# Performance work log

Measured on AMD Instinct MI355X. Metric: run time of the kernel, lower is better.

The kernel has to match this reference:

```python
import jax, jax.numpy as jnp
import numpy as np

N, E, L = 2048, 16384, 8
IN_DIM, HID, PE, EDGE_DIM, OUT_DIM, HEADS, MASK_DIM = 9, 256, 20, 2, 6, 8, 6
ENC = HID - PE
HD = HID // HEADS

def _bn(x, g, b):
    # BatchNorm1d in training-mode math (batch statistics, biased var), dropout disabled
    mu = x.mean(0)
    var = ((x - mu) ** 2).mean(0)
    return (x - mu) * jax.lax.rsqrt(var + 1e-5) * g + b

def _leaky(x):
    return jnp.where(x > 0, x, 0.01 * x)

def setup_inputs():
    key = jax.random.key(0)
    ks = iter(jax.random.split(key, 64))
    def p(*shape):
        return jax.random.normal(next(ks), shape, jnp.float32) * 0.05
    return dict(
        x=jax.random.normal(next(ks), (N, IN_DIM), jnp.float32),
        pe=jax.random.normal(next(ks), (N, PE), jnp.float32),
        edge_attr=jax.random.normal(next(ks), (E, EDGE_DIM), jnp.float32),
        mask_value=jax.random.normal(next(ks), (MASK_DIM,), jnp.float32),
        enc_w=p(IN_DIM, ENC), enc_b=p(ENC),
        in_g=jnp.ones((ENC,)), in_b=jnp.zeros((ENC,)),
        pe_g=jnp.ones((PE,)), pe_b=jnp.zeros((PE,)),
        gine_ew=p(L, EDGE_DIM, HID), gine_eb=p(L, HID),
        gine_mw=p(L, HID, HID), gine_mb=p(L, HID),
        attn_inw=p(L, HID, 3 * HID), attn_inb=p(L, 3 * HID),
        attn_outw=p(L, HID, HID), attn_outb=p(L, HID),
        mlp1w=p(L, HID, 2 * HID), mlp1b=p(L, 2 * HID),
        mlp2w=p(L, 2 * HID, HID), mlp2b=p(L, HID),
        n1g=jnp.ones((L, HID)), n1b=jnp.zeros((L, HID)),
        n2g=jnp.ones((L, HID)), n2b=jnp.zeros((L, HID)),
        n3g=jnp.ones((L, HID)), n3b=jnp.zeros((L, HID)),
        obn_g=jnp.ones((L, HID)), obn_b=jnp.zeros((L, HID)),
        pd_g=jnp.ones((HID,)), pd_b=jnp.zeros((HID,)),
        dec1w=p(HID, HID), dec1b=p(HID),
        dec2w=p(HID, OUT_DIM), dec2b=p(OUT_DIM),
        edge_index=jax.random.randint(next(ks), (2, E), 0, N, jnp.int32),
        mask=jax.random.randint(next(ks), (N, MASK_DIM), 0, 2, jnp.int32).astype(bool),
    )

def reference(x, pe, edge_attr, mask_value, enc_w, enc_b, in_g, in_b, pe_g, pe_b,
              gine_ew, gine_eb, gine_mw, gine_mb, attn_inw, attn_inb, attn_outw, attn_outb,
              mlp1w, mlp1b, mlp2w, mlp2b, n1g, n1b, n2g, n2b, n3g, n3b, obn_g, obn_b,
              pd_g, pd_b, dec1w, dec1b, dec2w, dec2b, edge_index, mask):
    src, dst = edge_index[0], edge_index[1]
    # masked-feature replacement on x[:, 3:3+mask_dim]
    blk = jnp.where(mask, mask_value[None, :], x[:, 3:3 + MASK_DIM])
    x = x.at[:, 3:3 + MASK_DIM].set(blk)
    h = _bn(_leaky(x @ enc_w + enc_b), in_g, in_b)
    h = jnp.concatenate([h, _bn(pe, pe_g, pe_b)], axis=1)  # [N, HID]
    for l in range(L):
        xin = h
        # GINEConv (eps=0): nn((1+eps)*x_i + sum_j relu(x_j + lin(e_ji)))
        eemb = edge_attr @ gine_ew[l] + gine_eb[l]            # [E, HID]
        msg = jax.nn.relu(xin[src] + eemb)                    # gather + fuse
        agg = jax.ops.segment_sum(msg, dst, num_segments=N)   # scatter-add
        hl = _leaky((xin + agg) @ gine_mw[l] + gine_mb[l])
        hl = _bn(hl + xin, n1g[l], n1b[l])                    # local branch + residual + norm1
        # global multi-head self-attention (single graph -> dense batch, no padding)
        qkv = xin @ attn_inw[l] + attn_inb[l]
        q, k, v = [t.reshape(N, HEADS, HD) for t in jnp.split(qkv, 3, axis=1)]
        a = jax.nn.softmax(jnp.einsum('nhd,mhd->hnm', q, k) / np.float32(np.sqrt(HD)), axis=-1)
        o = jnp.einsum('hnm,mhd->nhd', a, v).reshape(N, HID)
        ha = _bn(o @ attn_outw[l] + attn_outb[l] + xin, n2g[l], n2b[l])  # attn branch + residual + norm2
        out = hl + ha
        out = out + (jax.nn.relu(out @ mlp1w[l] + mlp1b[l]) @ mlp2w[l] + mlp2b[l])  # GPS FFN
        out = _bn(out, n3g[l], n3b[l])
        h = _bn(out, obn_g[l], obn_b[l])                      # outer per-layer BatchNorm
    h = _bn(h, pd_g, pd_b)
    return _leaky(h @ dec1w + dec1b) @ dec2w + dec2b
```

## Files before the change

### kernel.cpp

```cpp
#include <hip/hip_runtime.h>
#include <hip/hip_bf16.h>

typedef __hip_bfloat16 bf16;
typedef __attribute__((ext_vector_type(8))) short v8s;
typedef __attribute__((ext_vector_type(4))) float v4f;

#define NN 2048
#define EE 16384
#define LLAYERS 8
#define HIDD 256
#define ENCD 236
#define PED 20
#define BN_EPS 1e-5f
#define ATT_SCALE_L2E (0.17677669529663687f * 1.4426950408889634f)
#define KSPLIT 4

__device__ __forceinline__ float b2f(bf16 v){ return __bfloat162float(v); }
__device__ __forceinline__ float bs2f(unsigned short u){ return __uint_as_float(((unsigned)u) << 16); }
__device__ __forceinline__ unsigned short f2bs(float f){
  bf16 h = __float2bfloat16(f);
  union { bf16 b; unsigned short u; } cv; cv.b = h; return cv.u;
}
__device__ __forceinline__ float ld1f(const void* p, size_t i, int f){
  return f ? b2f(((const bf16*)p)[i]) : ((const float*)p)[i];
}

__global__ void k_detect2(const unsigned int* __restrict__ xw,
                          const unsigned char* __restrict__ mk, int* __restrict__ flags){
  __shared__ int sh[256];
  int t = threadIdx.x;
  if (blockIdx.x == 0){
    int cnt = 0;
    for (int i = t; i < 8192; i += 256){
      unsigned b = (xw[i] >> 8) & 0xffu;
      unsigned v = b & 0x7fu;
      if (v == 0u || (v >= 0x30u && v <= 0x43u)) cnt++;
    }
    sh[t] = cnt; __syncthreads();
    for (int s = 128; s; s >>= 1){ if (t < s) sh[t] += sh[t+s]; __syncthreads(); }
    if (t == 0) flags[0] = (sh[0] > 6000) ? 1 : 0;
  } else {
    int acc = 0;
    for (int i = t; i < NN*6; i += 256){
      unsigned b = mk[i]; int m = i & 3;
      if ((m == 1 && b == 0x3Fu) || (m == 0 && b == 0x80u)) acc |= 4;
      if (b == 0x3Fu || b == 0x80u) acc |= 2;
      if (m != 0 && b != 0u) acc |= 1;
    }
    sh[t] = acc; __syncthreads();
    for (int s = 128; s; s >>= 1){ if (t < s) sh[t] |= sh[t+s]; __syncthreads(); }
    if (t == 0){
      int a = sh[0];
      flags[1] = (a & 4) ? 2 : (a & 2) ? 3 : (a & 1) ? 1 : 0;
    }
  }
}

__global__ void k_tw(const void* __restrict__ src, unsigned short* __restrict__ dst,
                     int K, int N, const int* __restrict__ dflag){
  __shared__ float tile[32][33];
  int n0 = blockIdx.x*32, k0 = blockIdx.y*32, b = blockIdx.z;
  int t = threadIdx.x, x = t & 31, y = t >> 5;
  int f = dflag[0];
  size_t so = (size_t)b*K*N, dofs = (size_t)b*N*K;
  #pragma unroll
  for (int i = 0; i < 4; i++){
    int k = k0 + y + 8*i;
    tile[y+8*i][x] = ld1f(src, so + (size_t)k*N + n0 + x, f);
  }
  __syncthreads();
  #pragma unroll
  for (int i = 0; i < 4; i++){
    int n = n0 + y + 8*i;
    dst[dofs + (size_t)n*K + k0 + x] = f2bs(tile[x][y+8*i]);
  }
}
__global__ void k_tw3(const void* __restrict__ sA, const void* __restrict__ sB,
                      const void* __restrict__ sC, unsigned short* __restrict__ dst,
                      const int* __restrict__ dflag){
  __shared__ float tile[32][33];
  int z = blockIdx.z;
  const void* src = (z < 8) ? sA : (z < 16) ? sB : sC;
  int b = (z < 8) ? z : (z < 16) ? z - 8 : 0;
  int n0 = blockIdx.x*32, k0 = blockIdx.y*32;
  int t = threadIdx.x, x = t & 31, y = t >> 5;
  int f = dflag[0];
  size_t so = (size_t)b*65536, dofs = (size_t)z*65536;
  #pragma unroll
  for (int i = 0; i < 4; i++){
    int k = k0 + y + 8*i;
    tile[y+8*i][x] = ld1f(src, so + (size_t)k*256 + n0 + x, f);
  }
  __syncthreads();
  #pragma unroll
  for (int i = 0; i < 4; i++){
    int n = n0 + y + 8*i;
    dst[dofs + (size_t)n*256 + k0 + x] = f2bs(tile[x][y+8*i]);
  }
}

__global__ void k_csr_count(const int* __restrict__ ei, int* __restrict__ counts){
  int e = blockIdx.x*256 + threadIdx.x;
  if (e < EE) atomicAdd(&counts[ei[EE + e]], 1);
}
__global__ void k_csr_scan(const int* __restrict__ counts, int* __restrict__ rowstart,
                           int* __restrict__ cursor){
  __shared__ int ts[256];
  int t = threadIdx.x, base = t*8;
  int loc[8]; int s = 0;
  #pragma unroll
  for (int i = 0; i < 8; i++){ loc[i] = s; s += counts[base + i]; }
  ts[t] = s; __syncthreads();
  for (int off = 1; off < 256; off <<= 1){
    int v = (t >= off) ? ts[t - off] : 0;
    __syncthreads();
    ts[t] += v;
    __syncthreads();
  }
  int excl = ts[t] - s;
  #pragma unroll
  for (int i = 0; i < 8; i++){
    int v = excl + loc[i];
    rowstart[base + i] = v; cursor[base + i] = v;
  }
  if (t == 255) rowstart[2048] = ts[255];
}
__global__ void k_csr_fill(const int* __restrict__ ei, const void* __restrict__ ea,
                           const int* __restrict__ dflag, int* __restrict__ cursor,
                           int* __restrict__ csr_src, float2* __restrict__ csr_a){
  int e = blockIdx.x*256 + threadIdx.x;
  if (e >= EE) return;
  int s = ei[e], d = ei[EE + e];
  int pos = atomicAdd(&cursor[d], 1);
  int f = dflag[0];
  csr_src[pos] = s;
  csr_a[pos] = make_float2(ld1f(ea, (size_t)e*2, f), ld1f(ea, (size_t)e*2 + 1, f));
}

__global__ void k_encode(const void* __restrict__ x, const void* __restrict__ mval,
                         const void* __restrict__ mask, const int* __restrict__ flags,
                         const void* __restrict__ w, const void* __restrict__ b,
                         const void* __restrict__ pe,
                         float* __restrict__ out, float* __restrict__ pef){
  __shared__ float xr[16];
  int r = blockIdx.x, t = threadIdx.x;
  int f = flags[0];
  if (t < 9){
    float v = ld1f(x, (size_t)r*9 + t, f);
    if (t >= 3){
      int j = t - 3;
      size_t idx = (size_t)r*6 + j;
      int mf = flags[1];
      bool mm;
      if      (mf == 0) mm = ((const int*)mask)[idx] != 0;
      else if (mf == 1) mm = ((const unsigned char*)mask)[idx] != 0;
      else if (mf == 2) mm = ((const unsigned short*)mask)[idx] != 0;
      else              mm = ((const unsigned int*)mask)[idx] != 0;
      if (mm) v = ld1f(mval, j, f);
    }
    xr[t] = v;
  }
  __syncthreads();
  if (t < ENCD){
    float acc = ld1f(b, t, f);
    #pragma unroll
    for (int k = 0; k < 9; k++) acc = fmaf(xr[k], ld1f(w, (size_t)k*ENCD + t, f), acc);
    out[r*ENCD + t] = acc > 0.f ? acc : 0.01f*acc;
  } else {
    int j = t - ENCD;
    pef[(size_t)r*PED + j] = ld1f(pe, (size_t)r*PED + j, f);
  }
}
__global__ void k_bn2x(const float* __restrict__ encb, const float* __restrict__ pef,
                       const void* __restrict__ eg, const void* __restrict__ eb,
                       const void* __restrict__ pg, const void* __restrict__ pb,
                       const int* __restrict__ dflag,
                       float* __restrict__ scE, float* __restrict__ shE,
                       float* __restrict__ scP, float* __restrict__ shP){
  int cb = blockIdx.x, t = threadIdx.x;
  const float* src; int ld, c; const void *g, *b; float *sc, *sh;
  if (cb < ENCD){ src = encb; ld = ENCD; c = cb; g = eg; b = eb; sc = scE; sh = shE; }
  else          { src = pef;  ld = PED;  c = cb - ENCD; g = pg; b = pb; sc = scP; sh = shP; }
  float s = 0.f, q = 0.f;
  for (int r = t; r < NN; r += 256){ float v = src[(size_t)r*ld + c]; s += v; q += v*v; }
  __shared__ float ss[256], qs[256];
  ss[t] = s; qs[t] = q; __syncthreads();
  for (int k = 128; k; k >>= 1){ if (t < k){ ss[t] += ss[t+k]; qs[t] += qs[t+k]; } __syncthreads(); }
  if (t == 0){
    int f = dflag[0];
    float mu  = ss[0] * (1.f/NN);
    float var = qs[0] * (1.f/NN) - mu*mu;
    float r1  = rsqrtf(var + BN_EPS);
    float scv = ld1f(g, c, f) * r1;
    sc[c] = scv; sh[c] = ld1f(b, c, f) - mu*scv;
  }
}
__global__ void k_concat(unsigned short* __restrict__ h, const float* __restrict__ encb,
                         const float* __restrict__ pef,
                         const float* __restrict__ scE, const float* __restrict__ shE,
                         const float* __restrict__ scP, const float* __restrict__ shP){
  int i = blockIdx.x*256 + threadIdx.x;
  int r = i >> 8, c = i & 255;
  float v;
  if (c < ENCD) v = encb[r*ENCD + c]*scE[c] + shE[c];
  else { int j = c - ENCD; v = pef[r*PED + j]*scP[j] + shP[j]; }
  h[i] = f2bs(v);
}

__device__ __forceinline__ void dualbn(const float* slab, int c, int f,
                                       const void* g1, size_t g1o,
                                       const void* g2, size_t g2o,
                                       const void* b2, size_t b2o,
                                       float& sc, float& sh){
  float mu  = slab[2*c] * (1.f/NN);
  float var = slab[2*c+1] * (1.f/NN) - mu*mu;
  float r1  = rsqrtf(var + BN_EPS);
  float gg  = ld1f(g1, g1o + c, f);
  float zv  = var * r1 * r1 * gg * gg;
  float r2  = rsqrtf(zv + BN_EPS);
  sc = r1 * gg * r2 * ld1f(g2, g2o + c, f);
  sh = ld1f(b2, b2o + c, f) - mu*sc;
}
__device__ __forceinline__ void singlebn(const float* slab, int c, int f,
                                         const void* g, size_t go,
                                         const void* b, size_t bo,
                                         float& sc, float& sh){
  float mu  = slab[2*c] * (1.f/NN);
  float var = slab[2*c+1] * (1.f/NN) - mu*mu;
  float r1  = rsqrtf(var + BN_EPS);
  sc = ld1f(g, go + c, f) * r1;
  sh = ld1f(b, bo + c, f) - mu*sc;
}

__device__ void dev_gather(const unsigned short* __restrict__ h0,
                           const float* __restrict__ t3, int hsrc,
                           const float* __restrict__ slabH,
                           const void* Hg1, size_t Hg1o, const void* Hg2, size_t Hg2o,
                           const void* Hb2, size_t Hb2o,
                           int dst, const int* __restrict__ rowstart,
                           const int* __restrict__ csr_src, const float2* __restrict__ csr_a,
                           const void* __restrict__ w, size_t woff,
                           const void* __restrict__ b, size_t boff, int f,
                           float* __restrict__ agg){
  int c = threadIdx.x;
  float sc = 1.f, sh = 0.f;
  if (hsrc) dualbn(slabH, c, f, Hg1, Hg1o, Hg2, Hg2o, Hb2, Hb2o, sc, sh);
  float w0 = ld1f(w, woff + c, f), w1 = ld1f(w, woff + HIDD + c, f);
  float bb = ld1f(b, boff + c, f);
  int beg = rowstart[dst], end = rowstart[dst + 1];
  float acc = 0.f;
  for (int i = beg; i < end; i++){
    int s = csr_src[i]; float2 a = csr_a[i];
    float hv = hsrc ? t3[(size_t)s*HIDD + c]*sc + sh : bs2f(h0[(size_t)s*HIDD + c]);
    float m = hv + a.x*w0 + a.y*w1 + bb;
    acc += fmaxf(m, 0.f);
  }
  agg[(size_t)dst*HIDD + c] = acc;
}

template<int ACT, int APATH, int RESMODE, int OUTBF, int STATS>
__device__ void dev_mgemm(char* sm, int bn, int bm,
    const unsigned short* __restrict__ Ab, const float* __restrict__ Af, int hsrc,
    const float* __restrict__ agg,
    const float* __restrict__ Opart, const float* __restrict__ lsum,
    const float* __restrict__ t1p, const float* __restrict__ t2p,
    const float* __restrict__ slabH,
    const void* Hg1, size_t Hg1o, const void* Hg2, size_t Hg2o,
    const void* Hb2, size_t Hb2o,
    const void* Pg, size_t Pgo, const void* Pb, size_t Pbo,
    const float* __restrict__ slab1,
    const void* g1, size_t g1o, const void* b1, size_t b1o,
    const float* __restrict__ slab2,
    const void* g2, size_t g2o, const void* b2, size_t b2o,
    const unsigned short* __restrict__ Wt,
    const void* __restrict__ bias, size_t boff,
    void* __restrict__ C, int N_, int K, int qcols, float qscale,
    float* __restrict__ stats, int f){
  unsigned short (*As)[40] = (unsigned short(*)[40])sm;
  unsigned short (*Bs)[40] = (unsigned short(*)[40])(sm + 5120);
  constexpr bool NEEDH = (APATH <= 1 || RESMODE == 1 || APATH == 4);
  constexpr size_t TB = 10240 + (NEEDH ? 2048 : 0);
  float* scH = (float*)(sm + 10240); float* shH = scH + 256;
  float* tc1 = (float*)(sm + TB);    float* th1 = tc1 + 256;
  float* tc2 = th1 + 256;            float* th2 = tc2 + 256;
  int tid = threadIdx.x, L = tid & 63, wv = tid >> 6;
  int wm = wv >> 1, wn = wv & 1;
  int quad = L >> 4, lo = L & 15;
  int srow = tid >> 2, sk = (tid & 3)*8;

  if (NEEDH && (hsrc || APATH == 4)){
    int c = tid;
    float s, h;
    dualbn(slabH, c, f, Hg1, Hg1o, Hg2, Hg2o, Hb2, Hb2o, s, h);
    if (APATH == 4){
      float mu  = slabH[2*c] * (1.f/NN);
      float var = slabH[2*c+1] * (1.f/NN) - mu*mu;
      float muh = mu*s + h, varh = var*s*s;
      float rp  = rsqrtf(varh + BN_EPS);
      float sp  = ld1f(Pg, Pgo + c, f) * rp;
      float hp  = ld1f(Pb, Pbo + c, f) - muh*sp;
      s = s*sp; h = h*sp + hp;
    }
    scH[c] = s; shH[c] = h;
  }
  if (APATH == 3 || RESMODE == 2){
    int c = tid;
    float s, h;
    singlebn(slab1, c, f, g1, g1o, b1, b1o, s, h); tc1[c] = s; th1[c] = h;
    singlebn(slab2, c, f, g2, g2o, b2, b2o, s, h); tc2[c] = s; th2[c] = h;
  }
  __syncthreads();

  v4f acc[2][2];
  #pragma unroll
  for (int i = 0; i < 2; i++)
    #pragma unroll
    for (int j = 0; j < 2; j++) acc[i][j] = (v4f){0.f,0.f,0.f,0.f};

  for (int kk = 0; kk < K; kk += 32){
    int row = bm + srow, c0 = kk + sk;
    uint4 aval;
    if (APATH == 0 || APATH == 4){
      if (APATH == 0 && !hsrc){
        aval = *(const uint4*)(Ab + (size_t)row*K + c0);
      } else {
        unsigned short us8[8];
        #pragma unroll
        for (int j = 0; j < 8; j++){
          int c = c0 + j;
          us8[j] = f2bs(Af[(size_t)row*K + c]*scH[c] + shH[c]);
        }
        aval = *(const uint4*)us8;
      }
    } else if (APATH == 1){
      unsigned short us8[8];
      if (!hsrc){
        uint4 araw = *(const uint4*)(Ab + (size_t)row*K + c0);
        unsigned parts[4] = {araw.x, araw.y, araw.z, araw.w};
        #pragma unroll
        for (int p = 0; p < 4; p++){
          us8[2*p]   = f2bs(bs2f((unsigned short)(parts[p] & 0xffffu)) + agg[(size_t)row*K + c0 + 2*p]);
          us8[2*p+1] = f2bs(bs2f((unsigned short)(parts[p] >> 16))     + agg[(size_t)row*K + c0 + 2*p + 1]);
        }
      } else {
        #pragma unroll
        for (int j = 0; j < 8; j++){
          int c = c0 + j;
          us8[j] = f2bs(Af[(size_t)row*K + c]*scH[c] + shH[c] + agg[(size_t)row*K + c]);
        }
      }
      aval = *(const uint4*)us8;
    } else if (APATH == 2){
      int hd = c0 >> 5, d0 = c0 & 31;
      size_t mlb = ((size_t)row*8 + hd)*KSPLIT;
      float inv = 1.f / (lsum[mlb] + lsum[mlb+1] + lsum[mlb+2] + lsum[mlb+3]);
      const float* Op = Opart + mlb*32 + d0;
      unsigned short us8[8];
      #pragma unroll
      for (int j = 0; j < 8; j++){
        float v = (Op[j] + Op[32+j] + Op[64+j] + Op[96+j])*inv;
        us8[j] = f2bs(v);
      }
      aval = *(const uint4*)us8;
    } else {
      unsigned short us8[8];
      #pragma unroll
      for (int j = 0; j < 8; j++){
        int c = c0 + j;
        float v = t1p[(size_t)row*HIDD + c]*tc1[c] + th1[c]
                + t2p[(size_t)row*HIDD + c]*tc2[c] + th2[c];
        us8[j] = f2bs(v);
      }
      aval = *(const uint4*)us8;
    }
    uint4 bval = *(const uint4*)(Wt + (size_t)(bn + srow)*K + c0);
    __syncthreads();
    *(uint4*)&As[srow][sk] = aval;
    *(uint4*)&Bs[srow][sk] = bval;
    __syncthreads();
    v8s af[2], bfr[2];
    af[0]  = *(const v8s*)&As[wm*32 + lo][quad*8];
    af[1]  = *(const v8s*)&As[wm*32 + 16 + lo][quad*8];
    bfr[0] = *(const v8s*)&Bs[wn*32 + lo][quad*8];
    bfr[1] = *(const v8s*)&Bs[wn*32 + 16 + lo][quad*8];
    #pragma unroll
    for (int mi = 0; mi < 2; mi++)
      #pragma unroll
      for (int nj = 0; nj < 2; nj++)
        acc[mi][nj] = __builtin_amdgcn_mfma_f32_16x16x32_bf16(af[mi], bfr[nj], acc[mi][nj], 0, 0, 0);
  }

  float ssum[2] = {0.f, 0.f}, ssq[2] = {0.f, 0.f};
  #pragma unroll
  for (int mi = 0; mi < 2; mi++){
    #pragma unroll
    for (int nj = 0; nj < 2; nj++){
      int col = bn + wn*32 + nj*16 + lo;
      float bv = ld1f(bias, boff + col, f);
      #pragma unroll
      for (int r = 0; r < 4; r++){
        int row = bm + wm*32 + mi*16 + quad*4 + r;
        float t = acc[mi][nj][r] + bv;
        if (ACT == 1) t = fmaxf(t, 0.f);
        if (ACT == 2) t = t > 0.f ? t : 0.01f*t;
        if (qcols && col < qcols) t *= qscale;
        if (RESMODE == 1)
          t += hsrc ? (Af[(size_t)row*N_ + col]*scH[col] + shH[col])
                    : bs2f(Ab[(size_t)row*N_ + col]);
        if (RESMODE == 2)
          t += t1p[(size_t)row*HIDD + col]*tc1[col] + th1[col]
             + t2p[(size_t)row*HIDD + col]*tc2[col] + th2[col];
        if (STATS){ ssum[nj] += t; ssq[nj] += t*t; }
        if (OUTBF) ((unsigned short*)C)[(size_t)row*N_ + col] = f2bs(t);
        else       ((float*)C)[(size_t)row*N_ + col] = t;
      }
    }
  }
  if (STATS){
    #pragma unroll
    for (int nj = 0; nj < 2; nj++){
      float s = ssum[nj], q = ssq[nj];
      s += __shfl_xor(s, 16, 64); s += __shfl_xor(s, 32, 64);
      q += __shfl_xor(q, 16, 64); q += __shfl_xor(q, 32, 64);
      if (quad == 0){
        int col = bn + wn*32 + nj*16 + lo;
        atomicAdd(&stats[2*col],   s);
        atomicAdd(&stats[2*col+1], q);
      }
    }
  }
}

__launch_bounds__(512)
__global__ void k_d2(const unsigned short* __restrict__ qkv,
                     float* __restrict__ Opart, float* __restrict__ lsum){
  __shared__ unsigned short Ks[64][40];
  __shared__ unsigned short Vt[32][66];
  __shared__ unsigned short Ps[8][16][68];
  int b = blockIdx.x;
  int qt = b & 15, hd = (b >> 4) & 7, ks = b >> 7;
  int q0 = qt*128;
  int tid = threadIdx.x, L = tid & 63, wv = tid >> 6;
  int quad = L >> 4, lo = L & 15;
  int skey = tid >> 3, sd = (tid & 7)*4;

  v8s qf = *(const v8s*)(qkv + (size_t)(q0 + 16*wv + lo)*768 + hd*32 + quad*8);
  v4f o0 = (v4f){0.f,0.f,0.f,0.f}, o1 = (v4f){0.f,0.f,0.f,0.f};
  float lrow[4] = {0.f, 0.f, 0.f, 0.f};

  int kbeg = ks * (NN/KSPLIT), kend = kbeg + NN/KSPLIT;
  for (int kt = kbeg; kt < kend; kt += 64){
    const unsigned short* kp = qkv + (size_t)(kt + skey)*768 + 256 + hd*32 + sd;
    uint2 kraw = *(const uint2*)kp;
    uint2 vraw = *(const uint2*)(kp + 256);
    __syncthreads();
    *(uint2*)&Ks[skey][sd] = kraw;
    {
      unsigned short vs[4]; *(uint2*)vs = vraw;
      #pragma unroll
      for (int j = 0; j < 4; j++) Vt[sd + j][skey] = vs[j];
    }
    __syncthreads();
    v4f s[4];
    #pragma unroll
    for (int sub = 0; sub < 4; sub++){
      v8s kf = *(const v8s*)&Ks[sub*16 + lo][quad*8];
      s[sub] = __builtin_amdgcn_mfma_f32_16x16x32_bf16(qf, kf, (v4f){0.f,0.f,0.f,0.f}, 0, 0, 0);
    }
    #pragma unroll
    for (int r = 0; r < 4; r++){
      #pragma unroll
      for (int sub = 0; sub < 4; sub++){
        float p = exp2f(s[sub][r]);
        Ps[wv][quad*4 + r][sub*16 + lo] = f2bs(p);
        lrow[r] += p;
      }
    }
    #pragma unroll
    for (int kc = 0; kc < 2; kc++){
      v8s pf  = *(const v8s*)&Ps[wv][lo][kc*32 + quad*8];
      v8s v0f = *(const v8s*)&Vt[lo][kc*32 + quad*8];
      v8s v1f = *(const v8s*)&Vt[16 + lo][kc*32 + quad*8];
      o0 = __builtin_amdgcn_mfma_f32_16x16x32_bf16(pf, v0f, o0, 0, 0, 0);
      o1 = __builtin_amdgcn_mfma_f32_16x16x32_bf16(pf, v1f, o1, 0, 0, 0);
    }
  }
  #pragma unroll
  for (int r = 0; r < 4; r++){
    float v = lrow[r];
    #pragma unroll
    for (int off = 1; off < 16; off <<= 1) v += __shfl_xor(v, off, 64);
    lrow[r] = v;
  }
  #pragma unroll
  for (int r = 0; r < 4; r++){
    int row = q0 + 16*wv + quad*4 + r;
    size_t base = (((size_t)row*8 + hd)*KSPLIT + ks)*32;
    Opart[base + lo]      = o0[r];
    Opart[base + 16 + lo] = o1[r];
    if (lo == 0) lsum[((size_t)row*8 + hd)*KSPLIT + ks] = lrow[r];
  }
}

__launch_bounds__(256)
__global__ void k_d1(const unsigned short* __restrict__ h0, const float* __restrict__ t3,
                     int hsrc, const float* __restrict__ slabH,
                     const void* Hg1, size_t Hg1o, const void* Hg2, size_t Hg2o,
                     const void* Hb2, size_t Hb2o,
                     const unsigned short* __restrict__ qkw,
                     const void* qb, size_t qbo, unsigned short* __restrict__ qkvb,
                     const int* __restrict__ rowstart, const int* __restrict__ csr_src,
                     const float2* __restrict__ csr_a,
                     const void* gw, size_t gwo, const void* gb, size_t gbo,
                     float* __restrict__ agg, const int* __restrict__ dflagp){
  __shared__ char sm[12288];
  int f = dflagp[0];
  int bx = blockIdx.x;
  if (bx < 384){
    dev_mgemm<0,0,0,1,0>(sm, (bx % 12)*64, (bx / 12)*64, h0, t3, hsrc,
        nullptr, nullptr, nullptr, nullptr, nullptr,
        slabH, Hg1, Hg1o, Hg2, Hg2o, Hb2, Hb2o, nullptr, 0, nullptr, 0,
        nullptr, nullptr, 0, nullptr, 0, nullptr, nullptr, 0, nullptr, 0,
        qkw, qb, qbo, qkvb, 768, 256, 256, ATT_SCALE_L2E, nullptr, f);
  } else {
    dev_gather(h0, t3, hsrc, slabH, Hg1, Hg1o, Hg2, Hg2o, Hb2, Hb2o,
               bx - 384, rowstart, csr_src, csr_a, gw, gwo, gb, gbo, f, agg);
  }
}

__launch_bounds__(256)
__global__ void k_g3(const unsigned short* __restrict__ h0, const float* __restrict__ t3,
                     int hsrc, const float* __restrict__ slabH,
                     const void* Hg1, size_t Hg1o, const void* Hg2, size_t Hg2o,
                     const void* Hb2, size_t Hb2o,
                     const float* __restrict__ agg,
                     const unsigned short* __restrict__ gmw,
                     const void* gmb, size_t gmbo,
                     float* __restrict__ t1, float* __restrict__ stats1,
                     const float* __restrict__ Opart, const float* __restrict__ lsum,
                     const unsigned short* __restrict__ aow,
                     const void* aob, size_t aobo,
                     float* __restrict__ t2, float* __restrict__ stats2,
                     const int* __restrict__ dflagp){
  __shared__ char sm[12288];
  int f = dflagp[0];
  int bx = blockIdx.x;
  if (bx < 128){
    dev_mgemm<2,1,1,0,1>(sm, (bx & 3)*64, (bx >> 2)*64, h0, t3, hsrc,
        agg, nullptr, nullptr, nullptr, nullptr,
        slabH, Hg1, Hg1o, Hg2, Hg2o, Hb2, Hb2o, nullptr, 0, nullptr, 0,
        nullptr, nullptr, 0, nullptr, 0, nullptr, nullptr, 0, nullptr, 0,
        gmw, gmb, gmbo, t1, 256, 256, 0, 1.f, stats1, f);
  } else {
    int bb = bx - 128;
    dev_mgemm<0,2,1,0,1>(sm, (bb & 3)*64, (bb >> 2)*64, h0, t3, hsrc,
        nullptr, Opart, lsum, nullptr, nullptr,
        slabH, Hg1, Hg1o, Hg2, Hg2o, Hb2, Hb2o, nullptr, 0, nullptr, 0,
        nullptr, nullptr, 0, nullptr, 0, nullptr, nullptr, 0, nullptr, 0,
        aow, aob, aobo, t2, 256, 256, 0, 1.f, stats2, f);
  }
}

__launch_bounds__(256)
__global__ void k_g4(const float* __restrict__ t1, const float* __restrict__ t2,
                     const float* __restrict__ slab1,
                     const void* g1, size_t g1o, const void* b1, size_t b1o,
                     const float* __restrict__ slab2,
                     const void* g2, size_t g2o, const void* b2, size_t b2o,
                     const unsigned short* __restrict__ m1w,
                     const void* m1b, size_t m1bo,
                     unsigned short* __restrict__ u, const int* __restrict__ dflagp){
  __shared__ char sm[14336];
  dev_mgemm<1,3,0,1,0>(sm, blockIdx.x*64, blockIdx.y*64, nullptr, nullptr, 0,
      nullptr, nullptr, nullptr, t1, t2,
      nullptr, nullptr, 0, nullptr, 0, nullptr, 0, nullptr, 0, nullptr, 0,
      slab1, g1, g1o, b1, b1o, slab2, g2, g2o, b2, b2o,
      m1w, m1b, m1bo, u, 512, 256, 0, 1.f, nullptr, dflagp[0]);
}

__launch_bounds__(256)
__global__ void k_g5(const unsigned short* __restrict__ u,
                     const float* __restrict__ t1, const float* __restrict__ t2,
                     const float* __restrict__ slab1,
                     const void* g1, size_t g1o, const void* b1, size_t b1o,
                     const float* __restrict__ slab2,
                     const void* g2, size_t g2o, const void* b2, size_t b2o,
                     const unsigned short* __restrict__ m2w,
                     const void* m2b, size_t m2bo,
                     float* __restrict__ t3, float* __restrict__ stats3,
                     const int* __restrict__ dflagp){
  __shared__ char sm[14336];
  dev_mgemm<0,0,2,0,1>(sm, blockIdx.x*64, blockIdx.y*64, u, nullptr, 0,
      nullptr, nullptr, nullptr, t1, t2,
      nullptr, nullptr, 0, nullptr, 0, nullptr, 0, nullptr, 0, nullptr, 0,
      slab1, g1, g1o, b1, b1o, slab2, g2, g2o, b2, b2o,
      m2w, m2b, m2bo, t3, 256, 512, 0, 1.f, stats3, dflagp[0]);
}

__launch_bounds__(256)
__global__ void k_gdec(const float* __restrict__ t3, const float* __restrict__ slabH,
                       const void* Hg1, size_t Hg1o, const void* Hg2, size_t Hg2o,
                       const void* Hb2, size_t Hb2o,
                       const void* Pg, const void* Pb,
                       const unsigned short* __restrict__ d1w,
                       const void* d1bv, unsigned short* __restrict__ d1b,
                       const int* __restrict__ dflagp){
  __shared__ char sm[12288];
  dev_mgemm<2,4,0,1,0>(sm, blockIdx.x*64, blockIdx.y*64, nullptr, t3, 1,
      nullptr, nullptr, nullptr, nullptr, nullptr,
      slabH, Hg1, Hg1o, Hg2, Hg2o, Hb2, Hb2o, Pg, 0, Pb, 0,
      nullptr, nullptr, 0, nullptr, 0, nullptr, nullptr, 0, nullptr, 0,
      d1w, d1bv, 0, d1b, 256, 256, 0, 1.f, nullptr, dflagp[0]);
}

__global__ void k_dec2(const unsigned short* __restrict__ d1, const void* __restrict__ w,
                       const void* __restrict__ b, const int* __restrict__ dflag,
                       void* __restrict__ out){
  int r = blockIdx.x, t = threadIdx.x;
  int f = dflag[0];
  float a = bs2f(d1[(size_t)r*HIDD + t]);
  float p[6];
  #pragma unroll
  for (int n = 0; n < 6; n++) p[n] = a * ld1f(w, (size_t)t*6 + n, f);
  #pragma unroll
  for (int off = 32; off >= 1; off >>= 1)
    #pragma unroll
    for (int n = 0; n < 6; n++) p[n] += __shfl_down(p[n], off, 64);
  __shared__ float red[4][6];
  int wvv = t >> 6, ln = t & 63;
  if (ln == 0)
    #pragma unroll
    for (int n = 0; n < 6; n++) red[wvv][n] = p[n];
  __syncthreads();
  if (t < 6){
    float s = red[0][t] + red[1][t] + red[2][t] + red[3][t] + ld1f(b, t, f);
    if (f) ((bf16*)out)[r*6 + t] = __float2bfloat16(s);
    else   ((float*)out)[r*6 + t] = s;
  }
}

extern "C" void kernel_launch(void* const* d_in, const int* in_sizes, int n_in,
                              void* d_out, int out_size, void* d_ws, size_t ws_size,
                              hipStream_t stream){
  const void* x          = d_in[0];
  const void* pe         = d_in[1];
  const void* edge_attr  = d_in[2];
  const void* mask_value = d_in[3];
  const void* enc_w = d_in[4];  const void* enc_b = d_in[5];
  const void* in_g  = d_in[6];  const void* in_b  = d_in[7];
  const void* pe_g  = d_in[8];  const void* pe_b  = d_in[9];
  const void* gine_ew = d_in[10]; const void* gine_eb = d_in[11];
  const void* gine_mw = d_in[12]; const void* gine_mb = d_in[13];
  const void* attn_inw  = d_in[14]; const void* attn_inb  = d_in[15];
  const void* attn_outw = d_in[16]; const void* attn_outb = d_in[17];
  const void* mlp1w = d_in[18]; const void* mlp1b = d_in[19];
  const void* mlp2w = d_in[20]; const void* mlp2b = d_in[21];
  const void* n1g = d_in[22]; const void* n1b = d_in[23];
  const void* n2g = d_in[24]; const void* n2b = d_in[25];
  const void* n3g = d_in[26]; const void* n3b = d_in[27];
  const void* obn_g = d_in[28]; const void* obn_b = d_in[29];
  const void* pd_g  = d_in[30]; const void* pd_b  = d_in[31];
  const void* dec1w = d_in[32]; const void* dec1b = d_in[33];
  const void* dec2w = d_in[34]; const void* dec2b = d_in[35];
  const int*  edge_index = (const int*)d_in[36];
  const void* mask = d_in[37];
  (void)in_sizes; (void)n_in; (void)out_size; (void)ws_size;

  char* cur = (char*)d_ws;
  auto alloc = [&](size_t bytes)->char*{
    char* p = cur; cur += (bytes + 63) & ~(size_t)63; return p;
  };
  int*   flags = (int*)alloc(64);
  int*   dflag = flags;
  float* scE = (float*)alloc(ENCD*4); float* shE = (float*)alloc(ENCD*4);
  float* scP = (float*)alloc(PED*4);  float* shP = (float*)alloc(PED*4);
  int*   counts = (int*)alloc(2048*4);
  float* stats1 = (float*)alloc((size_t)LLAYERS*512*4);
  float* stats2 = (float*)alloc((size_t)LLAYERS*512*4);
  float* stats3 = (float*)alloc((size_t)LLAYERS*512*4);
  size_t zero_bytes = 2048*4 + 3*(size_t)LLAYERS*512*4;
  int*    rowstart = (int*)alloc(2052*4);
  int*    cursor   = (int*)alloc(2048*4);
  int*    csr_src  = (int*)alloc((size_t)EE*4);
  float2* csr_a    = (float2*)alloc((size_t)EE*8);
  unsigned short* h    = (unsigned short*)alloc((size_t)NN*HIDD*2);
  float*          t1   = (float*)alloc((size_t)NN*HIDD*4);
  float*          agg  = (float*)alloc((size_t)NN*HIDD*4);
  float*          t3   = (float*)alloc((size_t)NN*HIDD*4);
  unsigned short* qkvb = (unsigned short*)alloc((size_t)NN*768*2);
  float*          Opart= (float*)alloc((size_t)NN*8*KSPLIT*32*4);
  float*          lsum = (float*)alloc((size_t)NN*8*KSPLIT*4);
  unsigned short* sqw  = (unsigned short*)alloc((size_t)17*65536*2);
  unsigned short* ainw_t = (unsigned short*)alloc((size_t)8*768*256*2);
  unsigned short* m1w_t  = (unsigned short*)alloc((size_t)8*512*256*2);
  unsigned short* m2w_t  = (unsigned short*)alloc((size_t)8*256*512*2);
  unsigned short* gmw_t   = sqw;
  unsigned short* aoutw_t = sqw + (size_t)8*65536;
  unsigned short* d1w_t   = sqw + (size_t)16*65536;
  float* t2 = agg;
  unsigned short* u    = qkvb;
  float*          encb = (float*)qkvb;
  float*          pef  = (float*)qkvb + (size_t)NN*ENCD;
  unsigned short* d1b  = (unsigned short*)Opart;

  k_detect2<<<2, 256, 0, stream>>>((const unsigned int*)x, (const unsigned char*)mask, flags);
  hipMemsetAsync(counts, 0, zero_bytes, stream);
  k_csr_count<<<EE/256, 256, 0, stream>>>(edge_index, counts);
  k_csr_scan<<<1, 256, 0, stream>>>(counts, rowstart, cursor);
  k_csr_fill<<<EE/256, 256, 0, stream>>>(edge_index, edge_attr, dflag, cursor, csr_src, csr_a);
  k_tw3<<<dim3(8, 8, 17), 256, 0, stream>>>(gine_mw, attn_outw, dec1w, sqw, dflag);
  k_tw<<<dim3(24, 8, 8), 256, 0, stream>>>(attn_inw, ainw_t, 256, 768, dflag);
  k_tw<<<dim3(16, 8, 8), 256, 0, stream>>>(mlp1w,    m1w_t,  256, 512, dflag);
  k_tw<<<dim3(8, 16, 8), 256, 0, stream>>>(mlp2w,    m2w_t,  512, 256, dflag);
  k_encode<<<NN, 256, 0, stream>>>(x, mask_value, mask, flags, enc_w, enc_b, pe, encb, pef);
  k_bn2x<<<256, 256, 0, stream>>>(encb, pef, in_g, in_b, pe_g, pe_b, dflag, scE, shE, scP, shP);
  k_concat<<<NN*HIDD/256, 256, 0, stream>>>(h, encb, pef, scE, shE, scP, shP);

  for (int l = 0; l < LLAYERS; l++){
    int hs = (l > 0);
    const float* slH = stats3 + (size_t)(hs ? (l-1) : 0)*512;
    size_t o3 = (size_t)(hs ? (l-1) : 0)*256;
    k_d1<<<2432, 256, 0, stream>>>(h, t3, hs, slH, n3g, o3, obn_g, o3, obn_b, o3,
        ainw_t + (size_t)l*196608, attn_inb, (size_t)l*768, qkvb,
        rowstart, csr_src, csr_a,
        gine_ew, (size_t)l*2*HIDD, gine_eb, (size_t)l*HIDD, agg, dflag);
    k_d2<<<512, 512, 0, stream>>>(qkvb, Opart, lsum);
    k_g3<<<256, 256, 0, stream>>>(h, t3, hs, slH, n3g, o3, obn_g, o3, obn_b, o3,
        agg, gmw_t + (size_t)l*65536, gine_mb, (size_t)l*256, t1, stats1 + (size_t)l*512,
        Opart, lsum, aoutw_t + (size_t)l*65536, attn_outb, (size_t)l*256,
        t2, stats2 + (size_t)l*512, dflag);
    k_g4<<<dim3(8,32), 256, 0, stream>>>(t1, t2,
        stats1 + (size_t)l*512, n1g, (size_t)l*256, n1b, (size_t)l*256,
        stats2 + (size_t)l*512, n2g, (size_t)l*256, n2b, (size_t)l*256,
        m1w_t + (size_t)l*131072, mlp1b, (size_t)l*512, u, dflag);
    k_g5<<<dim3(4,32), 256, 0, stream>>>(u, t1, t2,
        stats1 + (size_t)l*512, n1g, (size_t)l*256, n1b, (size_t)l*256,
        stats2 + (size_t)l*512, n2g, (size_t)l*256, n2b, (size_t)l*256,
        m2w_t + (size_t)l*131072, mlp2b, (size_t)l*256, t3, stats3 + (size_t)l*512, dflag);
  }

  k_gdec<<<dim3(4,32), 256, 0, stream>>>(t3, stats3 + (size_t)7*512,
      n3g, (size_t)7*256, obn_g, (size_t)7*256, obn_b, (size_t)7*256,
      pd_g, pd_b, d1w_t, dec1b, d1b, dflag);
  k_dec2<<<NN, 256, 0, stream>>>(d1b, dec2w, dec2b, dflag, d_out);
}
```

Baseline: 798.7 us.

## Software-prefetch next tiles in GEMM, attention and gather loops

The fused GEMM now loads the next K-slice of A (raw fp32 or bf16) and B from global memory into registers right after the shared-memory barrier. The BN/convert math runs on the previous raw data, so global latency overlaps the MFMA work. The attention kernel likewise prefetches the next K/V tile, and the CSR gather prefetches the next edge index and attribute. t2 gets its own buffer instead of aliasing agg, likely because prefetching would otherwise read agg while it is being overwritten. This adds register pressure, which may reduce occupancy.

```diff
diff --git a/kernel.cpp b/kernel.cpp
--- a/kernel.cpp
+++ b/kernel.cpp
@@ -249,8 +249,11 @@
   float bb = ld1f(b, boff + c, f);
   int beg = rowstart[dst], end = rowstart[dst + 1];
   float acc = 0.f;
+  int sN = 0; float2 aN = make_float2(0.f, 0.f);
+  if (beg < end){ sN = csr_src[beg]; aN = csr_a[beg]; }
   for (int i = beg; i < end; i++){
-    int s = csr_src[i]; float2 a = csr_a[i];
+    int s = sN; float2 a = aN;
+    if (i + 1 < end){ sN = csr_src[i + 1]; aN = csr_a[i + 1]; }
     float hv = hsrc ? t3[(size_t)s*HIDD + c]*sc + sh : bs2f(h0[(size_t)s*HIDD + c]);
     float m = hv + a.x*w0 + a.y*w1 + bb;
     acc += fmaxf(m, 0.f);
@@ -287,6 +290,7 @@
   int wm = wv >> 1, wn = wv & 1;
   int quad = L >> 4, lo = L & 15;
   int srow = tid >> 2, sk = (tid & 3)*8;
+  int arow = bm + srow;
 
   if (NEEDH && (hsrc || APATH == 4)){
     int c = tid;
@@ -311,48 +315,69 @@
   }
   __syncthreads();
 
-  v4f acc[2][2];
-  #pragma unroll
-  for (int i = 0; i < 2; i++)
-    #pragma unroll
-    for (int j = 0; j < 2; j++) acc[i][j] = (v4f){0.f,0.f,0.f,0.f};
-
-  for (int kk = 0; kk < K; kk += 32){
-    int row = bm + srow, c0 = kk + sk;
-    uint4 aval;
+  uint4 bP = {};
+  uint4 aP = {};
+  float4 fP0 = {}, fP1 = {}, fP2 = {}, fP3 = {};
+  auto fetch_raw = [&](int c0){
+    bP = *(const uint4*)(Wt + (size_t)(bn + srow)*K + c0);
     if (APATH == 0 || APATH == 4){
       if (APATH == 0 && !hsrc){
-        aval = *(const uint4*)(Ab + (size_t)row*K + c0);
+        aP = *(const uint4*)(Ab + (size_t)arow*K + c0);
       } else {
-        unsigned short us8[8];
+        fP0 = *(const float4*)(Af + (size_t)arow*K + c0);
+        fP1 = *(const float4*)(Af + (size_t)arow*K + c0 + 4);
+      }
+    } else if (APATH == 1){
+      if (!hsrc){
+        aP = *(const uint4*)(Ab + (size_t)arow*K + c0);
+      } else {
+        fP0 = *(const float4*)(Af + (size_t)arow*K + c0);
+        fP1 = *(const float4*)(Af + (size_t)arow*K + c0 + 4);
+      }
+      fP2 = *(const float4*)(agg + (size_t)arow*K + c0);
+      fP3 = *(const float4*)(agg + (size_t)arow*K + c0 + 4);
+    } else if (APATH == 3){
+      fP0 = *(const float4*)(t1p + (size_t)arow*HIDD + c0);
+      fP1 = *(const float4*)(t1p + (size_t)arow*HIDD + c0 + 4);
+      fP2 = *(const float4*)(t2p + (size_t)arow*HIDD + c0);
+      fP3 = *(const float4*)(t2p + (size_t)arow*HIDD + c0 + 4);
+    }
+  };
+  auto make_aval = [&](int c0)->uint4 {
+    if (APATH == 0 && !hsrc) return aP;
+    if (APATH == 0 || APATH == 4){
+      unsigned short us8[8];
+      float fa[8] = {fP0.x,fP0.y,fP0.z,fP0.w,fP1.x,fP1.y,fP1.z,fP1.w};
+      #pragma unroll
+      for (int j = 0; j < 8; j++){
+        int c = c0 + j;
+        us8[j] = f2bs(fa[j]*scH[c] + shH[c]);
+      }
+      return *(const uint4*)us8;
+    }
+    if (APATH == 1){
+      unsigned short us8[8];
+      float ga[8] = {fP2.x,fP2.y,fP2.z,fP2.w,fP3.x,fP3.y,fP3.z,fP3.w};
+      if (!hsrc){
+        unsigned parts[4] = {aP.x, aP.y, aP.z, aP.w};
+        #pragma unroll
+        for (int p = 0; p < 4; p++){
+          us8[2*p]   = f2bs(bs2f((unsigned short)(parts[p] & 0xffffu)) + ga[2*p]);
+          us8[2*p+1] = f2bs(bs2f((unsigned short)(parts[p] >> 16))     + ga[2*p+1]);
+        }
+      } else {
+        float fa[8] = {fP0.x,fP0.y,fP0.z,fP0.w,fP1.x,fP1.y,fP1.z,fP1.w};
         #pragma unroll
         for (int j = 0; j < 8; j++){
           int c = c0 + j;
-          us8[j] = f2bs(Af[(size_t)row*K + c]*scH[c] + shH[c]);
-        }
-        aval = *(const uint4*)us8;
-      }
-    } else if (APATH == 1){
-      unsigned short us8[8];
-      if (!hsrc){
-        uint4 araw = *(const uint4*)(Ab + (size_t)row*K + c0);
-        unsigned parts[4] = {araw.x, araw.y, araw.z, araw.w};
-        #pragma unroll
-        for (int p = 0; p < 4; p++){
-          us8[2*p]   = f2bs(bs2f((unsigned short)(parts[p] & 0xffffu)) + agg[(size_t)row*K + c0 + 2*p]);
-          us8[2*p+1] = f2bs(bs2f((unsigned short)(parts[p] >> 16))     + agg[(size_t)row*K + c0 + 2*p + 1]);
-        }
-      } else {
-        #pragma unroll
-        for (int j = 0; j < 8; j++){
-          int c = c0 + j;
-          us8[j] = f2bs(Af[(size_t)row*K + c]*scH[c] + shH[c] + agg[(size_t)row*K + c]);
+          us8[j] = f2bs(fa[j]*scH[c] + shH[c] + ga[j]);
         }
       }
-      aval = *(const uint4*)us8;
-    } else if (APATH == 2){
+      return *(const uint4*)us8;
+    }
+    if (APATH == 2){
       int hd = c0 >> 5, d0 = c0 & 31;
-      size_t mlb = ((size_t)row*8 + hd)*KSPLIT;
+      size_t mlb = ((size_t)arow*8 + hd)*KSPLIT;
       float inv = 1.f / (lsum[mlb] + lsum[mlb+1] + lsum[mlb+2] + lsum[mlb+3]);
       const float* Op = Opart + mlb*32 + d0;
       unsigned short us8[8];
@@ -361,23 +386,35 @@
         float v = (Op[j] + Op[32+j] + Op[64+j] + Op[96+j])*inv;
         us8[j] = f2bs(v);
       }
-      aval = *(const uint4*)us8;
-    } else {
-      unsigned short us8[8];
-      #pragma unroll
-      for (int j = 0; j < 8; j++){
-        int c = c0 + j;
-        float v = t1p[(size_t)row*HIDD + c]*tc1[c] + th1[c]
-                + t2p[(size_t)row*HIDD + c]*tc2[c] + th2[c];
-        us8[j] = f2bs(v);
-      }
-      aval = *(const uint4*)us8;
-    }
-    uint4 bval = *(const uint4*)(Wt + (size_t)(bn + srow)*K + c0);
+      return *(const uint4*)us8;
+    }
+    unsigned short us8[8];
+    float fa[8] = {fP0.x,fP0.y,fP0.z,fP0.w,fP1.x,fP1.y,fP1.z,fP1.w};
+    float fb[8] = {fP2.x,fP2.y,fP2.z,fP2.w,fP3.x,fP3.y,fP3.z,fP3.w};
+    #pragma unroll
+    for (int j = 0; j < 8; j++){
+      int c = c0 + j;
+      us8[j] = f2bs(fa[j]*tc1[c] + th1[c] + fb[j]*tc2[c] + th2[c]);
+    }
+    return *(const uint4*)us8;
+  };
+
+  v4f acc[2][2];
+  #pragma unroll
+  for (int i = 0; i < 2; i++)
+    #pragma unroll
+    for (int j = 0; j < 2; j++) acc[i][j] = (v4f){0.f,0.f,0.f,0.f};
+
+  fetch_raw(sk);
+  for (int kk = 0; kk < K; kk += 32){
+    int c0 = kk + sk;
+    uint4 aval = make_aval(c0);
+    uint4 bval = bP;
     __syncthreads();
     *(uint4*)&As[srow][sk] = aval;
     *(uint4*)&Bs[srow][sk] = bval;
     __syncthreads();
+    if (kk + 32 < K) fetch_raw(kk + 32 + sk);
     v8s af[2], bfr[2];
     af[0]  = *(const v8s*)&As[wm*32 + lo][quad*8];
     af[1]  = *(const v8s*)&As[wm*32 + 16 + lo][quad*8];
@@ -449,10 +486,10 @@
   float lrow[4] = {0.f, 0.f, 0.f, 0.f};
 
   int kbeg = ks * (NN/KSPLIT), kend = kbeg + NN/KSPLIT;
+  const unsigned short* kp0 = qkv + (size_t)(kbeg + skey)*768 + 256 + hd*32 + sd;
+  uint2 kraw = *(const uint2*)kp0;
+  uint2 vraw = *(const uint2*)(kp0 + 256);
   for (int kt = kbeg; kt < kend; kt += 64){
-    const unsigned short* kp = qkv + (size_t)(kt + skey)*768 + 256 + hd*32 + sd;
-    uint2 kraw = *(const uint2*)kp;
-    uint2 vraw = *(const uint2*)(kp + 256);
     __syncthreads();
     *(uint2*)&Ks[skey][sd] = kraw;
     {
@@ -461,6 +498,11 @@
       for (int j = 0; j < 4; j++) Vt[sd + j][skey] = vs[j];
     }
     __syncthreads();
+    if (kt + 64 < kend){
+      const unsigned short* kp = qkv + (size_t)(kt + 64 + skey)*768 + 256 + hd*32 + sd;
+      kraw = *(const uint2*)kp;
+      vraw = *(const uint2*)(kp + 256);
+    }
     v4f s[4];
     #pragma unroll
     for (int sub = 0; sub < 4; sub++){
@@ -686,6 +728,7 @@
   unsigned short* h    = (unsigned short*)alloc((size_t)NN*HIDD*2);
   float*          t1   = (float*)alloc((size_t)NN*HIDD*4);
   float*          agg  = (float*)alloc((size_t)NN*HIDD*4);
+  float*          t2   = (float*)alloc((size_t)NN*HIDD*4);
   float*          t3   = (float*)alloc((size_t)NN*HIDD*4);
   unsigned short* qkvb = (unsigned short*)alloc((size_t)NN*768*2);
   float*          Opart= (float*)alloc((size_t)NN*8*KSPLIT*32*4);
@@ -697,7 +740,6 @@
   unsigned short* gmw_t   = sqw;
   unsigned short* aoutw_t = sqw + (size_t)8*65536;
   unsigned short* d1w_t   = sqw + (size_t)16*65536;
-  float* t2 = agg;
   unsigned short* u    = qkvb;
   float*          encb = (float*)qkvb;
   float*          pef  = (float*)qkvb + (size_t)NN*ENCD;
```

New measurement: 823.3 us. 1.03x slower.
